# Performance work log

Hardware: AMD Instinct MI355X
Metric: run time of the kernel (lower is better)

## Reference

```python
import jax, jax.numpy as jnp
from jax import lax
import numpy as np

D_MODEL = 1024
D_STATE = 16
D_CONV = 4
EXPAND = 2
D_INNER = EXPAND * D_MODEL  # 2048
DT_RANK = D_MODEL // 16     # 64
EPS = 1e-5


def _ln(x, g, b):
    mu = jnp.mean(x, axis=-1, keepdims=True)
    var = jnp.mean(jnp.square(x - mu), axis=-1, keepdims=True)
    return (x - mu) * lax.rsqrt(var + EPS) * g + b


def setup_inputs() -> dict:
    key = jax.random.key(0)
    ks = jax.random.split(key, 16)
    B, L = 2, 1024
    s = 0.02  # weight init scale
    inp = {
        'x': jax.random.normal(ks[0], (B, L, D_MODEL), jnp.float32),
        'n1_g': jnp.ones((D_MODEL,), jnp.float32),
        'n1_b': jnp.zeros((D_MODEL,), jnp.float32),
        'n2_g': jnp.ones((D_MODEL,), jnp.float32),
        'n2_b': jnp.zeros((D_MODEL,), jnp.float32),
        'in_proj_w': jax.random.normal(ks[1], (2 * D_INNER, D_MODEL), jnp.float32) * s,
        'conv_w': jax.random.normal(ks[2], (D_INNER, 1, D_CONV), jnp.float32) * 0.1,
        'conv_b': jnp.zeros((D_INNER,), jnp.float32),
        'x_proj_w': jax.random.normal(ks[3], (DT_RANK + 2 * D_STATE, D_INNER), jnp.float32) * s,
        'dt_w': jax.random.normal(ks[4], (D_INNER, DT_RANK), jnp.float32) * s,
        'dt_b': jnp.full((D_INNER,), -4.0, jnp.float32) + jax.random.normal(ks[5], (D_INNER,), jnp.float32) * 0.1,
        'A_log': jnp.tile(jnp.log(jnp.arange(1, D_STATE + 1, dtype=jnp.float32))[None, :], (D_INNER, 1)),
        'D': jnp.ones((D_INNER,), jnp.float32),
        'out_w': jax.random.normal(ks[6], (D_MODEL, D_INNER), jnp.float32) * s,
        'ffg_w': jax.random.normal(ks[7], (2 * D_MODEL, D_MODEL), jnp.float32) * s,
        'ffg_b': jnp.zeros((2 * D_MODEL,), jnp.float32),
        'ffp_w': jax.random.normal(ks[8], (D_MODEL, D_MODEL), jnp.float32) * s,
        'ffp_b': jnp.zeros((D_MODEL,), jnp.float32),
    }
    return inp


def _mamba(u, in_proj_w, conv_w, conv_b, x_proj_w, dt_w, dt_b, A_log, D, out_w):
    Bsz, L, _ = u.shape
    xz = u @ in_proj_w.T                      # [B,L,2*Di]
    x_in, z = jnp.split(xz, 2, axis=-1)
    # depthwise causal conv over time
    xc = x_in.transpose(0, 2, 1)              # [B,Di,L]
    xc = lax.conv_general_dilated(
        xc, conv_w, window_strides=(1,), padding=[(D_CONV - 1, 0)],
        dimension_numbers=('NCH', 'OIH', 'NCH'), feature_group_count=D_INNER)
    xc = jax.nn.silu(xc + conv_b[None, :, None]).transpose(0, 2, 1)  # [B,L,Di]
    # input-dependent SSM params
    x_dbl = xc @ x_proj_w.T                   # [B,L,dt_rank+2*N]
    dt, Bm, Cm = jnp.split(x_dbl, [DT_RANK, DT_RANK + D_STATE], axis=-1)
    delta = jax.nn.softplus(dt @ dt_w.T + dt_b)        # [B,L,Di]
    A = -jnp.exp(A_log)                                # [Di,N]
    dA = jnp.exp(jnp.einsum('bld,dn->bldn', delta, A))   # [B,L,Di,N]
    dBu = jnp.einsum('bld,bln,bld->bldn', delta, Bm, xc)  # [B,L,Di,N]

    def step(h, inp):
        dA_t, dBu_t, C_t = inp
        h = dA_t * h + dBu_t                  # [B,Di,N]
        y = jnp.einsum('bdn,bn->bd', h, C_t)
        return h, y

    h0 = jnp.zeros((Bsz, D_INNER, D_STATE), u.dtype)
    _, ys = lax.scan(step, h0, (dA.transpose(1, 0, 2, 3),
                                dBu.transpose(1, 0, 2, 3),
                                Cm.transpose(1, 0, 2)))
    y = ys.transpose(1, 0, 2) + xc * D        # skip via D
    y = y * jax.nn.silu(z)                    # output gate
    return y @ out_w.T


def reference(x, n1_g, n1_b, n2_g, n2_b, in_proj_w, conv_w, conv_b, x_proj_w,
              dt_w, dt_b, A_log, D, out_w, ffg_w, ffg_b, ffp_w, ffp_b):
    # x = x + ssm(norm1(x))
    x = x + _mamba(_ln(x, n1_g, n1_b), in_proj_w, conv_w, conv_b, x_proj_w,
                   dt_w, dt_b, A_log, D, out_w)
    # gated FFN residual
    normed = _ln(x, n2_g, n2_b)
    gate, val = jnp.split(normed @ ffg_w.T + ffg_b, 2, axis=-1)
    x = x + (jax.nn.silu(gate) * val) @ ffp_w.T + ffp_b
    return x
```

## Files before the change

### kernel.cpp

```cpp
#include <hip/hip_runtime.h>
#include <hip/hip_bf16.h>

#define DM 1024
#define DI 2048
#define LSEQ 1024
#define BSZ 2
#define NROWS (BSZ*LSEQ)
#define NC 32
#define CL 32

typedef __attribute__((ext_vector_type(4))) float f32x4;
typedef __attribute__((ext_vector_type(8))) short bf16x8;
typedef __hip_bfloat16 bf16;

__device__ __forceinline__ float sigmoidf_(float x){ return 1.f/(1.f+__expf(-x)); }

__global__ void cvt_kernel(const float* __restrict__ src, bf16* __restrict__ dst,
                           long n, int cols, int src_stride, int src_rows)
{
  long i = (long)blockIdx.x*blockDim.x + threadIdx.x;
  if (i >= n) return;
  int r = (int)(i / cols);
  int c = (int)(i - (long)r*cols);
  float v = (r < src_rows) ? src[(long)r*src_stride + c] : 0.f;
  dst[i] = __float2bfloat16(v);
}

__global__ __launch_bounds__(256) void ln_kernel(const float* __restrict__ x,
    const float* __restrict__ g, const float* __restrict__ b, bf16* __restrict__ out)
{
  int row = blockIdx.x;
  float4 v = ((const float4*)(x + (long)row*DM))[threadIdx.x];
  float s  = v.x+v.y+v.z+v.w;
  float s2 = v.x*v.x+v.y*v.y+v.z*v.z+v.w*v.w;
  #pragma unroll
  for (int m=32;m;m>>=1){ s += __shfl_xor(s,m); s2 += __shfl_xor(s2,m); }
  __shared__ float ws0[4], ws1[4];
  int wv = threadIdx.x>>6;
  if ((threadIdx.x&63)==0){ ws0[wv]=s; ws1[wv]=s2; }
  __syncthreads();
  s  = ws0[0]+ws0[1]+ws0[2]+ws0[3];
  s2 = ws1[0]+ws1[1]+ws1[2]+ws1[3];
  float mu  = s*(1.f/DM);
  float var = s2*(1.f/DM) - mu*mu;
  float rs  = rsqrtf(var + 1e-5f);
  int c = threadIdx.x*4;
  float4 gg = ((const float4*)g)[threadIdx.x];
  float4 bb = ((const float4*)b)[threadIdx.x];
  bf16* o = out + (long)row*DM + c;
  o[0] = __float2bfloat16((v.x-mu)*rs*gg.x + bb.x);
  o[1] = __float2bfloat16((v.y-mu)*rs*gg.y + bb.y);
  o[2] = __float2bfloat16((v.z-mu)*rs*gg.z + bb.z);
  o[3] = __float2bfloat16((v.w-mu)*rs*gg.w + bb.w);
}

template<int ACT>
__global__ __launch_bounds__(256)
void gemm_k(const short* __restrict__ A, int lda, const short* __restrict__ B, int ldb,
            int K, int Nreal, int ldo, int pstride,
            const float* __restrict__ bias, const float* __restrict__ res,
            float* __restrict__ outf, bf16* __restrict__ outb)
{
  A += (size_t)blockIdx.z * K;
  B += (size_t)blockIdx.z * K;
  if (outf) outf += (size_t)blockIdx.z * pstride;

  __shared__ short As[128*32];
  __shared__ short Bs[128*32];
  const int tid  = threadIdx.x;
  const int wave = tid>>6, lane = tid&63;
  const int m0 = blockIdx.x*128, n0 = blockIdx.y*128;
  const int wm = (wave>>1)*64, wn = (wave&1)*64;
  const int lr = lane&15, lk = lane>>4;

  f32x4 acc[4][4];
  #pragma unroll
  for (int i=0;i<4;i++)
    #pragma unroll
    for (int j=0;j<4;j++) acc[i][j] = f32x4{0.f,0.f,0.f,0.f};

  const int r0 = tid>>2;
  const int kb = (tid&3)*8;

  for (int kt=0; kt<K; kt+=32) {
    #pragma unroll
    for (int i=0;i<2;i++){
      int row = r0 + i*64;
      __builtin_amdgcn_global_load_lds(
        (const __attribute__((address_space(1))) void*)(A + (size_t)(m0+row)*lda + kt + kb),
        (__attribute__((address_space(3))) void*)(As + row*32 + kb), 16, 0, 0);
    }
    #pragma unroll
    for (int i=0;i<2;i++){
      int row = r0 + i*64;
      __builtin_amdgcn_global_load_lds(
        (const __attribute__((address_space(1))) void*)(B + (size_t)(n0+row)*ldb + kt + kb),
        (__attribute__((address_space(3))) void*)(Bs + row*32 + kb), 16, 0, 0);
    }
    asm volatile("s_waitcnt vmcnt(0)");
    __syncthreads();
    bf16x8 af[4], bfr[4];
    #pragma unroll
    for (int i=0;i<4;i++) af[i]  = *(const bf16x8*)(As + (wm+i*16+lr)*32 + lk*8);
    #pragma unroll
    for (int j=0;j<4;j++) bfr[j] = *(const bf16x8*)(Bs + (wn+j*16+lr)*32 + lk*8);
    #pragma unroll
    for (int i=0;i<4;i++)
      #pragma unroll
      for (int j=0;j<4;j++)
        acc[i][j] = __builtin_amdgcn_mfma_f32_16x16x32_bf16(af[i], bfr[j], acc[i][j], 0,0,0);
    __syncthreads();
  }

  #pragma unroll
  for (int i=0;i<4;i++){
    #pragma unroll
    for (int j=0;j<4;j++){
      int col = n0 + wn + j*16 + lr;
      if (col >= Nreal) continue;
      #pragma unroll
      for (int r=0;r<4;r++){
        int row = m0 + wm + i*16 + lk*4 + r;
        float v = acc[i][j][r];
        if (bias) v += bias[col];
        if (ACT==1){
          float ev = __expf(v);
          v = (v > 20.f) ? v : __logf(1.f + ev);
        }
        if (res)  v += res[(size_t)row*ldo + col];
        if (outf) outf[(size_t)row*ldo + col] = v;
        if (outb) outb[(size_t)row*ldo + col] = __float2bfloat16(v);
      }
    }
  }
}

__global__ __launch_bounds__(256) void xproj_reduce(const float* __restrict__ part,
    float* __restrict__ xdbl, bf16* __restrict__ dt16)
{
  int i = blockIdx.x*256 + threadIdx.x;
  if (i >= NROWS*96) return;
  float s = 0.f;
  #pragma unroll
  for (int k=0;k<8;k++) s += part[(long)k*(NROWS*96) + i];
  xdbl[i] = s;
  int r = i/96, c = i - r*96;
  if (c < 64) dt16[r*64 + c] = __float2bfloat16(s);
}

__global__ __launch_bounds__(256) void conv_kernel(const bf16* __restrict__ xz,
    const float* __restrict__ w, const float* __restrict__ cb,
    float* __restrict__ xcf, bf16* __restrict__ xcb)
{
  long i = (long)blockIdx.x*blockDim.x + threadIdx.x;
  int d  = (int)(i & (DI-1));
  int bl = (int)(i >> 11);
  int l  = bl & (LSEQ-1);
  int b  = bl >> 10;
  float acc = cb[d];
  #pragma unroll
  for (int k=0;k<4;k++){
    int ls = l-3+k;
    if (ls >= 0)
      acc += __bfloat162float(xz[(long)(b*LSEQ+ls)*(2*DI) + d]) * w[d*4+k];
  }
  float s = acc * sigmoidf_(acc);
  xcf[i] = s;
  xcb[i] = __float2bfloat16(s);
}


#define H16(du, duxv, B0,B1,B2,B3) \
  h0  = __expf((du)*An0 )*h0  + (duxv)*(B0).x; \
  h1  = __expf((du)*An1 )*h1  + (duxv)*(B0).y; \
  h2  = __expf((du)*An2 )*h2  + (duxv)*(B0).z; \
  h3  = __expf((du)*An3 )*h3  + (duxv)*(B0).w; \
  h4  = __expf((du)*An4 )*h4  + (duxv)*(B1).x; \
  h5  = __expf((du)*An5 )*h5  + (duxv)*(B1).y; \
  h6  = __expf((du)*An6 )*h6  + (duxv)*(B1).z; \
  h7  = __expf((du)*An7 )*h7  + (duxv)*(B1).w; \
  h8  = __expf((du)*An8 )*h8  + (duxv)*(B2).x; \
  h9  = __expf((du)*An9 )*h9  + (duxv)*(B2).y; \
  h10 = __expf((du)*An10)*h10 + (duxv)*(B2).z; \
  h11 = __expf((du)*An11)*h11 + (duxv)*(B2).w; \
  h12 = __expf((du)*An12)*h12 + (duxv)*(B3).x; \
  h13 = __expf((du)*An13)*h13 + (duxv)*(B3).y; \
  h14 = __expf((du)*An14)*h14 + (duxv)*(B3).z; \
  h15 = __expf((du)*An15)*h15 + (duxv)*(B3).w;

#define DECL_AN(Alog_ptr, d) \
  float4 al0 = ((const float4*)((Alog_ptr) + (d)*16))[0]; \
  float4 al1 = ((const float4*)((Alog_ptr) + (d)*16))[1]; \
  float4 al2 = ((const float4*)((Alog_ptr) + (d)*16))[2]; \
  float4 al3 = ((const float4*)((Alog_ptr) + (d)*16))[3]; \
  float An0=-__expf(al0.x), An1=-__expf(al0.y), An2 =-__expf(al0.z), An3 =-__expf(al0.w); \
  float An4=-__expf(al1.x), An5=-__expf(al1.y), An6 =-__expf(al1.z), An7 =-__expf(al1.w); \
  float An8=-__expf(al2.x), An9=-__expf(al2.y), An10=-__expf(al2.z), An11=-__expf(al2.w); \
  float An12=-__expf(al3.x),An13=-__expf(al3.y),An14=-__expf(al3.z), An15=-__expf(al3.w);

__global__ __launch_bounds__(256) void scan_p1(
    const float* __restrict__ delta, const float* __restrict__ xc,
    const float* __restrict__ xdbl, const float* __restrict__ A_log,
    float* __restrict__ S, float* __restrict__ sumDu)
{
  const int tid = threadIdx.x;
  const int d   = blockIdx.x*256 + tid;
  const int c   = blockIdx.y, b = blockIdx.z;
  const int bd  = b*2048 + d;
  DECL_AN(A_log, d);
  __shared__ float sB[CL][16];
  {
    int e = tid*2;
    int r = e>>4, n = e&15;
    long row = (long)b*LSEQ + c*CL + r;
    sB[r][n]   = xdbl[row*96 + 64 + n];
    sB[r][n+1] = xdbl[row*96 + 64 + n+1];
  }
  __syncthreads();
  float h0=0,h1=0,h2=0,h3=0,h4=0,h5=0,h6=0,h7=0,
        h8=0,h9=0,h10=0,h11=0,h12=0,h13=0,h14=0,h15=0;
  float sdu = 0.f;
  const long rbase = (long)b*LSEQ + c*CL;
  #pragma unroll
  for (int s0=0; s0<CL; s0+=8){
    float du8[8], xv8[8];
    #pragma unroll
    for (int i=0;i<8;i++){
      long row = rbase + s0 + i;
      du8[i] = delta[row*DI + d];
      xv8[i] = xc[row*DI + d];
    }
    #pragma unroll
    for (int i=0;i<8;i++){
      float du = du8[i], duxv = du*xv8[i];
      sdu += du;
      const float4* bb = (const float4*)sB[s0+i];
      float4 B0=bb[0], B1=bb[1], B2=bb[2], B3=bb[3];
      H16(du, duxv, B0,B1,B2,B3);
    }
  }
  sumDu[c*4096 + bd] = sdu;
  float hs[16] = {h0,h1,h2,h3,h4,h5,h6,h7,h8,h9,h10,h11,h12,h13,h14,h15};
  #pragma unroll
  for (int n=0;n<16;n++) S[(c*16+n)*4096 + bd] = hs[n];
}

__global__ __launch_bounds__(256) void scan_p2(const float* __restrict__ S,
    const float* __restrict__ sumDu, const float* __restrict__ A_log,
    float* __restrict__ hin)
{
  int t = blockIdx.x*256 + threadIdx.x;
  int n = t >> 12, bd = t & 4095;
  int d = bd & 2047;
  float Aneg = -__expf(A_log[d*16 + n]);
  float h = 0.f;
  #pragma unroll
  for (int c=0;c<NC;c++){
    hin[(c*16+n)*4096 + bd] = h;
    float P = __expf(Aneg * sumDu[c*4096 + bd]);
    h = S[(c*16+n)*4096 + bd] + P*h;
  }
}

__global__ __launch_bounds__(256) void scan_p3(
    const float* __restrict__ delta, const float* __restrict__ xc,
    const float* __restrict__ xdbl, const bf16* __restrict__ xz,
    const float* __restrict__ A_log, const float* __restrict__ Dp,
    const float* __restrict__ hin, bf16* __restrict__ y)
{
  const int tid = threadIdx.x;
  const int d   = blockIdx.x*256 + tid;
  const int c   = blockIdx.y, b = blockIdx.z;
  const int bd  = b*2048 + d;
  DECL_AN(A_log, d);
  const float Dd = Dp[d];
  __shared__ float sB[CL][16], sC[CL][16];
  {
    int e = tid*2;
    int r = e>>4, n = e&15;
    long row = (long)b*LSEQ + c*CL + r;
    sB[r][n]   = xdbl[row*96 + 64 + n];
    sB[r][n+1] = xdbl[row*96 + 64 + n+1];
    sC[r][n]   = xdbl[row*96 + 80 + n];
    sC[r][n+1] = xdbl[row*96 + 80 + n+1];
  }
  __syncthreads();
  float h0,h1,h2,h3,h4,h5,h6,h7,h8,h9,h10,h11,h12,h13,h14,h15;
  {
    const float* hp = hin + c*16*4096 + bd;
    h0 =hp[0];       h1 =hp[4096];    h2 =hp[2*4096];  h3 =hp[3*4096];
    h4 =hp[4*4096];  h5 =hp[5*4096];  h6 =hp[6*4096];  h7 =hp[7*4096];
    h8 =hp[8*4096];  h9 =hp[9*4096];  h10=hp[10*4096]; h11=hp[11*4096];
    h12=hp[12*4096]; h13=hp[13*4096]; h14=hp[14*4096]; h15=hp[15*4096];
  }
  const long rbase = (long)b*LSEQ + c*CL;
  #pragma unroll
  for (int s0=0; s0<CL; s0+=8){
    float du8[8], xv8[8], zv8[8];
    #pragma unroll
    for (int i=0;i<8;i++){
      long row = rbase + s0 + i;
      du8[i] = delta[row*DI + d];
      xv8[i] = xc[row*DI + d];
      zv8[i] = __bfloat162float(xz[row*(2*DI) + DI + d]);
    }
    #pragma unroll
    for (int i=0;i<8;i++){
      float du = du8[i], xv = xv8[i], duxv = du*xv;
      const float4* bb = (const float4*)sB[s0+i];
      float4 B0=bb[0], B1=bb[1], B2=bb[2], B3=bb[3];
      H16(du, duxv, B0,B1,B2,B3);
      const float4* cc = (const float4*)sC[s0+i];
      float4 C0=cc[0], C1=cc[1], C2=cc[2], C3=cc[3];
      float r0 = h0*C0.x + h4*C1.x + h8 *C2.x + h12*C3.x;
      float r1 = h1*C0.y + h5*C1.y + h9 *C2.y + h13*C3.y;
      float r2 = h2*C0.z + h6*C1.z + h10*C2.z + h14*C3.z;
      float r3 = h3*C0.w + h7*C1.w + h11*C2.w + h15*C3.w;
      float r = (r0+r1) + (r2+r3) + xv*Dd;
      float z = zv8[i];
      y[(rbase+s0+i)*DI + d] = __float2bfloat16(r * (z*sigmoidf_(z)));
    }
  }
}

__global__ __launch_bounds__(256) void gated_kernel(const float* __restrict__ gv,
                                                    bf16* __restrict__ g)
{
  long i = (long)blockIdx.x*blockDim.x + threadIdx.x;
  int r = (int)(i >> 10);
  int c = (int)(i & (DM-1));
  float gt = gv[(long)r*(2*DM) + c];
  float vl = gv[(long)r*(2*DM) + DM + c];
  g[i] = __float2bfloat16(gt * sigmoidf_(gt) * vl);
}

extern "C" void kernel_launch(void* const* d_in, const int* in_sizes, int n_in,
                              void* d_out, int out_size, void* d_ws, size_t ws_size,
                              hipStream_t stream)
{
  const float* x        = (const float*)d_in[0];
  const float* n1_g     = (const float*)d_in[1];
  const float* n1_b     = (const float*)d_in[2];
  const float* n2_g     = (const float*)d_in[3];
  const float* n2_b     = (const float*)d_in[4];
  const float* in_proj_w= (const float*)d_in[5];
  const float* conv_w   = (const float*)d_in[6];
  const float* conv_b   = (const float*)d_in[7];
  const float* x_proj_w = (const float*)d_in[8];
  const float* dt_w     = (const float*)d_in[9];
  const float* dt_b     = (const float*)d_in[10];
  const float* A_log    = (const float*)d_in[11];
  const float* Dp       = (const float*)d_in[12];
  const float* out_w    = (const float*)d_in[13];
  const float* ffg_w    = (const float*)d_in[14];
  const float* ffg_b    = (const float*)d_in[15];
  const float* ffp_w    = (const float*)d_in[16];
  const float* ffp_b    = (const float*)d_in[17];

  char* ws = (char*)d_ws;
  bf16* w_inproj = (bf16*)(ws + 0);
  bf16* w_xproj  = (bf16*)(ws + 8388608);
  bf16* w_dt     = (bf16*)(ws + 8912896);
  bf16* w_out    = (bf16*)(ws + 9175040);
  bf16* w_ffg    = (bf16*)(ws + 13369344);
  bf16* w_ffp    = (bf16*)(ws + 17563648);
  bf16* x1_b     = (bf16*)(ws + 19660800);
  bf16* xz_b     = (bf16*)(ws + 23855104);
  bf16* xc_b     = (bf16*)(ws + 40632320);
  float* S_buf   = (float*)(ws + 40632320);
  float* sumDu   = (float*)(ws + 8388608);
  bf16* dt16     = (bf16*)(ws + 49020928);
  bf16* y_b      = (bf16*)(ws + 49283072);
  float* xc_f    = (float*)(ws + 57671680);
  float* xdbl_f  = (float*)(ws + 74448896);
  float* delta_f = (float*)(ws + 75235328);
  float* part_xp = (float*)(ws + 75235328);
  float* x2_f    = (float*)(ws + 92012544);
  float* hin     = (float*)(ws + 92012544);
  float* outp    = (float*)d_out;

  #define GRID1(n) dim3((int)(((n)+255)/256))
  cvt_kernel<<<GRID1(4096L*1024), 256, 0, stream>>>(in_proj_w, w_inproj, 4096L*1024, 1024, 1024, 4096);
  cvt_kernel<<<GRID1(128L*2048), 256, 0, stream>>>(x_proj_w,  w_xproj,  128L*2048, 2048, 2048, 96);
  cvt_kernel<<<GRID1(2048L*64),  256, 0, stream>>>(dt_w,      w_dt,     2048L*64,   64,   64, 2048);
  cvt_kernel<<<GRID1(1024L*2048),256, 0, stream>>>(out_w,     w_out,    1024L*2048, 2048, 2048, 1024);
  cvt_kernel<<<GRID1(2048L*1024),256, 0, stream>>>(ffg_w,     w_ffg,    2048L*1024, 1024, 1024, 2048);
  cvt_kernel<<<GRID1(1024L*1024),256, 0, stream>>>(ffp_w,     w_ffp,    1024L*1024, 1024, 1024, 1024);

  ln_kernel<<<NROWS, 256, 0, stream>>>(x, n1_g, n1_b, x1_b);
  gemm_k<0><<<dim3(16,32), 256, 0, stream>>>((const short*)x1_b, 1024, (const short*)w_inproj, 1024,
      1024, 4096, 4096, 0, nullptr, nullptr, nullptr, xz_b);
  conv_kernel<<<GRID1((long)NROWS*DI), 256, 0, stream>>>(xz_b, conv_w, conv_b, xc_f, xc_b);
  gemm_k<0><<<dim3(16,1,8), 256, 0, stream>>>((const short*)xc_b, 2048, (const short*)w_xproj, 2048,
      256, 96, 96, NROWS*96, nullptr, nullptr, part_xp, nullptr);
  xproj_reduce<<<GRID1((long)NROWS*96), 256, 0, stream>>>(part_xp, xdbl_f, dt16);
  gemm_k<1><<<dim3(16,16), 256, 0, stream>>>((const short*)dt16, 64, (const short*)w_dt, 64,
      64, 2048, 2048, 0, dt_b, nullptr, delta_f, nullptr);
  scan_p1<<<dim3(8,NC,2), 256, 0, stream>>>(delta_f, xc_f, xdbl_f, A_log, S_buf, sumDu);
  scan_p2<<<dim3(256), 256, 0, stream>>>(S_buf, sumDu, A_log, hin);
  scan_p3<<<dim3(8,NC,2), 256, 0, stream>>>(delta_f, xc_f, xdbl_f, xz_b, A_log, Dp, hin, y_b);
  gemm_k<0><<<dim3(16,8), 256, 0, stream>>>((const short*)y_b, 2048, (const short*)w_out, 2048,
      2048, 1024, 1024, 0, nullptr, x, x2_f, nullptr);
  ln_kernel<<<NROWS, 256, 0, stream>>>(x2_f, n2_g, n2_b, x1_b);
  gemm_k<0><<<dim3(16,16), 256, 0, stream>>>((const short*)x1_b, 1024, (const short*)w_ffg, 1024,
      1024, 2048, 2048, 0, ffg_b, nullptr, delta_f, nullptr);
  gated_kernel<<<GRID1((long)NROWS*DM), 256, 0, stream>>>(delta_f, y_b);
  gemm_k<0><<<dim3(16,8), 256, 0, stream>>>((const short*)y_b, 1024, (const short*)w_ffp, 1024,
      1024, 1024, 1024, 0, ffp_b, x2_f, outp, nullptr);
  #undef GRID1
}
```

Baseline: 432.7 us.

## Double-buffer GEMM LDS tiles and split-K the out and FFN-projection GEMMs

```diff
diff --git a/kernel.cpp b/kernel.cpp
--- a/kernel.cpp
+++ b/kernel.cpp
@@ -65,8 +65,8 @@
   B += (size_t)blockIdx.z * K;
   if (outf) outf += (size_t)blockIdx.z * pstride;
 
-  __shared__ short As[128*32];
-  __shared__ short Bs[128*32];
+  __shared__ short As[2][128*32];
+  __shared__ short Bs[2][128*32];
   const int tid  = threadIdx.x;
   const int wave = tid>>6, lane = tid&63;
   const int m0 = blockIdx.x*128, n0 = blockIdx.y*128;
@@ -81,36 +81,41 @@
 
   const int r0 = tid>>2;
   const int kb = (tid&3)*8;
-
-  for (int kt=0; kt<K; kt+=32) {
-    #pragma unroll
-    for (int i=0;i<2;i++){
-      int row = r0 + i*64;
-      __builtin_amdgcn_global_load_lds(
-        (const __attribute__((address_space(1))) void*)(A + (size_t)(m0+row)*lda + kt + kb),
-        (__attribute__((address_space(3))) void*)(As + row*32 + kb), 16, 0, 0);
-    }
-    #pragma unroll
-    for (int i=0;i<2;i++){
-      int row = r0 + i*64;
-      __builtin_amdgcn_global_load_lds(
-        (const __attribute__((address_space(1))) void*)(B + (size_t)(n0+row)*ldb + kt + kb),
-        (__attribute__((address_space(3))) void*)(Bs + row*32 + kb), 16, 0, 0);
-    }
-    asm volatile("s_waitcnt vmcnt(0)");
-    __syncthreads();
+  const short* Arow = A + (size_t)(m0+r0)*lda + kb;
+  const short* Brow = B + (size_t)(n0+r0)*ldb + kb;
+
+#define STAGE_T(buf, kt) do { \
+    __builtin_amdgcn_global_load_lds((const __attribute__((address_space(1))) void*)(Arow + (kt)), \
+        (__attribute__((address_space(3))) void*)(&As[buf][r0*32+kb]), 16, 0, 0); \
+    __builtin_amdgcn_global_load_lds((const __attribute__((address_space(1))) void*)(Arow + (size_t)64*lda + (kt)), \
+        (__attribute__((address_space(3))) void*)(&As[buf][(r0+64)*32+kb]), 16, 0, 0); \
+    __builtin_amdgcn_global_load_lds((const __attribute__((address_space(1))) void*)(Brow + (kt)), \
+        (__attribute__((address_space(3))) void*)(&Bs[buf][r0*32+kb]), 16, 0, 0); \
+    __builtin_amdgcn_global_load_lds((const __attribute__((address_space(1))) void*)(Brow + (size_t)64*ldb + (kt)), \
+        (__attribute__((address_space(3))) void*)(&Bs[buf][(r0+64)*32+kb]), 16, 0, 0); \
+  } while(0)
+
+  STAGE_T(0, 0);
+  asm volatile("s_waitcnt vmcnt(0)");
+  __syncthreads();
+  int cur = 0;
+  for (int kt = 32; kt <= K; kt += 32) {
+    if (kt < K) STAGE_T(cur^1, kt);
     bf16x8 af[4], bfr[4];
     #pragma unroll
-    for (int i=0;i<4;i++) af[i]  = *(const bf16x8*)(As + (wm+i*16+lr)*32 + lk*8);
-    #pragma unroll
-    for (int j=0;j<4;j++) bfr[j] = *(const bf16x8*)(Bs + (wn+j*16+lr)*32 + lk*8);
+    for (int i=0;i<4;i++) af[i]  = *(const bf16x8*)(&As[cur][(wm+i*16+lr)*32 + lk*8]);
+    #pragma unroll
+    for (int j=0;j<4;j++) bfr[j] = *(const bf16x8*)(&Bs[cur][(wn+j*16+lr)*32 + lk*8]);
     #pragma unroll
     for (int i=0;i<4;i++)
       #pragma unroll
       for (int j=0;j<4;j++)
         acc[i][j] = __builtin_amdgcn_mfma_f32_16x16x32_bf16(af[i], bfr[j], acc[i][j], 0,0,0);
+    asm volatile("s_waitcnt vmcnt(0)");
     __syncthreads();
-  }
+    cur ^= 1;
+  }
+#undef STAGE_T
 
   #pragma unroll
   for (int i=0;i<4;i++){
@@ -133,6 +138,26 @@
       }
     }
   }
+}
+
+__global__ __launch_bounds__(256) void red2_kernel(
+    const float* __restrict__ p0, const float* __restrict__ p1,
+    const float* __restrict__ bias, const float* __restrict__ res,
+    float* __restrict__ outf)
+{
+  long i = ((long)blockIdx.x*256 + threadIdx.x)*4;
+  float4 a = *(const float4*)(p0+i);
+  float4 b = *(const float4*)(p1+i);
+  float4 o = {a.x+b.x, a.y+b.y, a.z+b.z, a.w+b.w};
+  if (bias){
+    const float4 bb = *(const float4*)(bias + (int)(i & (DM-1)));
+    o.x+=bb.x; o.y+=bb.y; o.z+=bb.z; o.w+=bb.w;
+  }
+  if (res){
+    float4 r = *(const float4*)(res+i);
+    o.x+=r.x; o.y+=r.y; o.z+=r.z; o.w+=r.w;
+  }
+  *(float4*)(outf+i) = o;
 }
 
 __global__ __launch_bounds__(256) void xproj_reduce(const float* __restrict__ part,
@@ -366,6 +391,7 @@
   bf16* w_ffp    = (bf16*)(ws + 17563648);
   bf16* x1_b     = (bf16*)(ws + 19660800);
   bf16* xz_b     = (bf16*)(ws + 23855104);
+  float* part_fp = (float*)(ws + 23855104);
   bf16* xc_b     = (bf16*)(ws + 40632320);
   float* S_buf   = (float*)(ws + 40632320);
   float* sumDu   = (float*)(ws + 8388608);
@@ -375,6 +401,7 @@
   float* xdbl_f  = (float*)(ws + 74448896);
   float* delta_f = (float*)(ws + 75235328);
   float* part_xp = (float*)(ws + 75235328);
+  float* part_op = (float*)(ws + 75235328);
   float* x2_f    = (float*)(ws + 92012544);
   float* hin     = (float*)(ws + 92012544);
   float* outp    = (float*)d_out;
@@ -399,13 +426,15 @@
   scan_p1<<<dim3(8,NC,2), 256, 0, stream>>>(delta_f, xc_f, xdbl_f, A_log, S_buf, sumDu);
   scan_p2<<<dim3(256), 256, 0, stream>>>(S_buf, sumDu, A_log, hin);
   scan_p3<<<dim3(8,NC,2), 256, 0, stream>>>(delta_f, xc_f, xdbl_f, xz_b, A_log, Dp, hin, y_b);
-  gemm_k<0><<<dim3(16,8), 256, 0, stream>>>((const short*)y_b, 2048, (const short*)w_out, 2048,
-      2048, 1024, 1024, 0, nullptr, x, x2_f, nullptr);
+  gemm_k<0><<<dim3(16,8,2), 256, 0, stream>>>((const short*)y_b, 2048, (const short*)w_out, 2048,
+      1024, 1024, 1024, NROWS*DM, nullptr, nullptr, part_op, nullptr);
+  red2_kernel<<<dim3(2048), 256, 0, stream>>>(part_op, part_op + (long)NROWS*DM, nullptr, x, x2_f);
   ln_kernel<<<NROWS, 256, 0, stream>>>(x2_f, n2_g, n2_b, x1_b);
   gemm_k<0><<<dim3(16,16), 256, 0, stream>>>((const short*)x1_b, 1024, (const short*)w_ffg, 1024,
       1024, 2048, 2048, 0, ffg_b, nullptr, delta_f, nullptr);
   gated_kernel<<<GRID1((long)NROWS*DM), 256, 0, stream>>>(delta_f, y_b);
-  gemm_k<0><<<dim3(16,8), 256, 0, stream>>>((const short*)y_b, 1024, (const short*)w_ffp, 1024,
-      1024, 1024, 1024, 0, ffp_b, x2_f, outp, nullptr);
+  gemm_k<0><<<dim3(16,8,2), 256, 0, stream>>>((const short*)y_b, 1024, (const short*)w_ffp, 1024,
+      512, 1024, 1024, NROWS*DM, nullptr, nullptr, part_fp, nullptr);
+  red2_kernel<<<dim3(2048), 256, 0, stream>>>(part_fp, part_fp + (long)NROWS*DM, ffp_b, x2_f, outp);
   #undef GRID1
 }
```

After: 375.0 us. 1.15x faster.
